# Optimization experiments

Hardware: AMD Instinct MI355X
Metric: run time of the kernel (lower is better)

The kernel has to match this reference:

```python
import jax, jax.numpy as jnp
import numpy as np

B = 262144      # points per batch
DIM = 3         # input_dim
L = 16          # levels
T = 19          # log2 hash table size
F = 2           # features per level
N_MIN, N_MAX = 16, 512

_b = np.exp((np.log(N_MAX) - np.log(N_MIN)) / (L - 1))
RES = np.floor(N_MIN * _b ** np.arange(L)).astype(np.float32).reshape(1, 1, L, 1)

# voxel corner offsets [1, DIM, 1, 2^DIM]
_border = np.empty((DIM, 2 ** DIM), dtype=np.uint32)
for i in range(DIM):
    _border[i, :] = np.array(([0] * 2 ** i + [1] * 2 ** i) * 2 ** (DIM - i - 1), dtype=np.uint32)
BORDER = _border.reshape(1, DIM, 1, 2 ** DIM)

# tiny-cuda-nn hash primes; all fit in uint32. Since the torch code takes the
# result mod 2^T (a power of two), int64 and uint32 arithmetic agree on the
# low bits, so uint32 hashing is bit-exact with the original.
PRIMES = np.array([1, 2654435761, 805459861], dtype=np.uint32)
MASK = np.uint32(2 ** T - 1)


def setup_inputs() -> dict:
    key = jax.random.key(0)
    k1, k2 = jax.random.split(key)
    x = jax.random.uniform(k1, (B, DIM), dtype=jnp.float32)  # coords in [0,1)
    tables = jax.random.uniform(k2, (L, 2 ** T, F), dtype=jnp.float32,
                                minval=-1e-4, maxval=1e-4)
    return {"x": x, "tables": tables}


def reference(x, tables):
    res = jnp.asarray(RES)                                   # [1,1,L,1]
    border = jnp.asarray(BORDER)                             # [1,DIM,1,2^DIM]
    primes = jnp.asarray(PRIMES)
    scaled = x[:, :, None, None] * res                       # [B,DIM,L,1]
    grid = jnp.floor(scaled).astype(jnp.uint32) + border     # [B,DIM,L,2^DIM]
    # spatial hash: xor of per-dim coord * prime, mod 2^T
    h = (grid[:, 0] * primes[0]) ^ (grid[:, 1] * primes[1]) ^ (grid[:, 2] * primes[2])
    idx = (h & MASK).astype(jnp.int32)                       # [B,L,2^DIM]
    gathered = tables[jnp.arange(L)[None, :, None], idx]     # [B,L,2^DIM,F]
    # multilinear interpolation weights
    w = jnp.prod(1.0 - jnp.abs(scaled - grid.astype(scaled.dtype)), axis=1)  # [B,L,2^DIM]
    out = jnp.einsum('blv,blvf->blf', w, gathered)           # [B,L,F]
    return out.reshape(x.shape[0], L * F)
```

## Files before the change

### kernel.cpp

```cpp
#include <hip/hip_runtime.h>


#define NB 262144
#define NL 16
#define TSIZE (1u << 19)
#define TMASK ((1u << 19) - 1u)
#define P1 2654435761u
#define P2 805459861u

typedef float vf2 __attribute__((ext_vector_type(2)));
typedef float vf4 __attribute__((ext_vector_type(4)));

__constant__ float RES_C[NL] = {16.f, 20.f, 25.f, 32.f, 40.f, 50.f, 64.f, 80.f,
                                101.f, 128.f, 161.f, 203.f, 256.f, 322.f, 406.f, 512.f};

__device__ __forceinline__ void ngp_point_level(
    float px, float py, float pz, int l, const float* __restrict__ tables,
    float& o0, float& o1) {
  const float res = RES_C[l];
  const float sx = px * res, sy = py * res, sz = pz * res;
  const float fx = floorf(sx), fy = floorf(sy), fz = floorf(sz);
  const unsigned ix = (unsigned)fx, iy = (unsigned)fy, iz = (unsigned)fz;

  const unsigned hy0 = iy * P1, hy1 = hy0 + P1;
  const unsigned hz0 = iz * P2, hz1 = hz0 + P2;

  const float wx0 = 1.0f - fabsf(sx - fx);
  const float wx1 = 1.0f - fabsf(sx - (fx + 1.0f));
  const float wy0 = 1.0f - fabsf(sy - fy);
  const float wy1 = 1.0f - fabsf(sy - (fy + 1.0f));
  const float wz0 = 1.0f - fabsf(sz - fz);
  const float wz1 = 1.0f - fabsf(sz - (fz + 1.0f));

  const vf2* __restrict__ tbl2 = (const vf2*)tables + (size_t)l * TSIZE;
  const vf4* __restrict__ tbl4 = (const vf4*)tables + (size_t)l * (TSIZE / 2);

  unsigned hyz[4];
  hyz[0] = hy0 ^ hz0;
  hyz[1] = hy1 ^ hz0;
  hyz[2] = hy0 ^ hz1;
  hyz[3] = hy1 ^ hz1;

  vf2 g[8];
  if ((ix & 1u) == 0u) {
#pragma unroll
    for (int p = 0; p < 4; ++p) {
      const unsigned i0 = (ix ^ hyz[p]) & TMASK;
      const vf4 q = tbl4[i0 >> 1];
      vf2 lo; lo.x = q.x; lo.y = q.y;
      vf2 hi; hi.x = q.z; hi.y = q.w;
      const bool x0_is_lo = (i0 & 1u) == 0u;
      g[2 * p + 0] = x0_is_lo ? lo : hi;
      g[2 * p + 1] = x0_is_lo ? hi : lo;
    }
  } else {
#pragma unroll
    for (int p = 0; p < 4; ++p) {
      const unsigned i0 = (ix ^ hyz[p]) & TMASK;
      const unsigned i1 = ((ix + 1u) ^ hyz[p]) & TMASK;
      g[2 * p + 0] = tbl2[i0];
      g[2 * p + 1] = tbl2[i1];
    }
  }

  o0 = 0.0f; o1 = 0.0f;
#pragma unroll
  for (int v = 0; v < 8; ++v) {
    const float w = ((v & 1) ? wx1 : wx0) * ((v & 2) ? wy1 : wy0) * ((v & 4) ? wz1 : wz0);
    o0 = fmaf(w, g[v].x, o0);
    o1 = fmaf(w, g[v].y, o1);
  }
}

__global__ __launch_bounds__(256) void ngp_gather_kernel(
    const float* __restrict__ x,
    const float* __restrict__ tables,
    vf2* __restrict__ ws) {
  const int i = blockIdx.x;
  const int lvl = (i & 7) | ((i >> 13) << 3);
  const int chunk = (i >> 3) & 1023;
  const int b = chunk * 256 + threadIdx.x;

  const float px = __builtin_nontemporal_load(x + b * 3 + 0);
  const float py = __builtin_nontemporal_load(x + b * 3 + 1);
  const float pz = __builtin_nontemporal_load(x + b * 3 + 2);

  float o0, o1;
  ngp_point_level(px, py, pz, lvl, tables, o0, o1);

  vf2 r; r.x = o0; r.y = o1;
  __builtin_nontemporal_store(r, ws + (size_t)lvl * NB + b);
}

__global__ __launch_bounds__(256) void ngp_transpose_kernel(
    const vf2* __restrict__ ws,
    vf4* __restrict__ out4) {
  __shared__ vf2 tile[NL][257];
  const int t = threadIdx.x;
  const int p0 = blockIdx.x * 256;

#pragma unroll
  for (int l = 0; l < NL; ++l) {
    tile[l][t] = __builtin_nontemporal_load(ws + (size_t)l * NB + p0 + t);
  }
  __syncthreads();

#pragma unroll
  for (int k = 0; k < 8; ++k) {
    const int q = k * 256 + t;
    const int pq = q >> 3;
    const int wq = q & 7;
    const vf2 a = tile[2 * wq + 0][pq];
    const vf2 c = tile[2 * wq + 1][pq];
    vf4 v; v.x = a.x; v.y = a.y; v.z = c.x; v.w = c.y;
    __builtin_nontemporal_store(v, out4 + (size_t)p0 * 8 + q);
  }
}

__global__ __launch_bounds__(256) void ngp_fused_kernel(
    const float* __restrict__ x, const float* __restrict__ tables,
    float* __restrict__ out) {
  const int tid = blockIdx.x * blockDim.x + threadIdx.x;
  const int l = tid & (NL - 1);
  const int b = tid >> 4;
  float o0, o1;
  ngp_point_level(x[b * 3], x[b * 3 + 1], x[b * 3 + 2], l, tables, o0, o1);
  float2 r = make_float2(o0, o1);
  ((float2*)out)[tid] = r;
}

extern "C" void kernel_launch(void* const* d_in, const int* in_sizes, int n_in,
                              void* d_out, int out_size, void* d_ws, size_t ws_size,
                              hipStream_t stream) {
  const float* x = (const float*)d_in[0];
  const float* tables = (const float*)d_in[1];
  float* out = (float*)d_out;

  const size_t ws_needed = (size_t)NL * NB * sizeof(vf2);
  if (ws_size >= ws_needed) {
    vf2* ws = (vf2*)d_ws;
    ngp_gather_kernel<<<NB * NL / 256, 256, 0, stream>>>(x, tables, ws);
    ngp_transpose_kernel<<<NB / 256, 256, 0, stream>>>(ws, (vf4*)out);
  } else {
    ngp_fused_kernel<<<NB * NL / 256, 256, 0, stream>>>(x, tables, out);
  }
}
```

Baseline: 197.7 us.

## Cache dense coarse-level grids in LDS and remap blocks per XCD

For the three coarsest levels, the block loads every grid vertex (up to 26^3) from the hash table into shared memory once, then serves 8192 points' corner lookups from LDS instead of global random gathers. The remaining levels keep the global gather path. Blocks grow to 1024 threads and are assigned so each XCD sees contiguous level/chunk work, aiming at better L2 locality per table. The cost is a large LDS footprint (~140KB) that limits occupancy, plus prefill work that is redundant across the 32 chunks of each coarse level.

```diff
diff --git a/kernel.cpp b/kernel.cpp
--- a/kernel.cpp
+++ b/kernel.cpp
@@ -7,6 +7,16 @@
 #define TMASK ((1u << 19) - 1u)
 #define P1 2654435761u
 #define P2 805459861u
+
+#define NCL 3
+#define LDS_ENT (26 * 26 * 26)
+#define CPTS 8192
+#define CBLKS (NB / CPTS)
+#define CB_PER_XCD ((NCL * CBLKS) / 8)
+#define FINE_CHUNKS 256
+#define FINE_TOTAL ((NL - NCL) * FINE_CHUNKS)
+#define FINE_PER_XCD (FINE_TOTAL / 8)
+#define GRID_BLOCKS (8 * (CB_PER_XCD + FINE_PER_XCD))
 
 typedef float vf2 __attribute__((ext_vector_type(2)));
 typedef float vf4 __attribute__((ext_vector_type(4)));
@@ -72,14 +82,101 @@
   }
 }
 
-__global__ __launch_bounds__(256) void ngp_gather_kernel(
+template <int E>
+__device__ __forceinline__ void coarse_block(
+    const int lvl, const int cchunk, const float* __restrict__ x,
+    const float* __restrict__ tables, vf2* __restrict__ ws,
+    vf2* __restrict__ cache) {
+  const int tid = threadIdx.x;
+  const vf4* __restrict__ tbl4 = (const vf4*)tables + (size_t)lvl * (TSIZE / 2);
+
+  constexpr int HE = (E + 1) / 2;
+  constexpr int U = HE * E * E;
+
+  for (int u = tid; u < U; u += 1024) {
+    const int iz = u / (HE * E);
+    const int rem = u - iz * (HE * E);
+    const int iy = rem / HE;
+    const int ixh = rem - iy * HE;
+    const unsigned ix = 2u * (unsigned)ixh;
+    const unsigned h0 = (ix ^ ((unsigned)iy * P1) ^ ((unsigned)iz * P2)) & TMASK;
+    const vf4 q = tbl4[h0 >> 1];
+    vf2 lo; lo.x = q.x; lo.y = q.y;
+    vf2 hi; hi.x = q.z; hi.y = q.w;
+    const bool x0_is_lo = (h0 & 1u) == 0u;
+    const int d0 = (int)ix + E * (iy + E * iz);
+    cache[d0] = x0_is_lo ? lo : hi;
+    if ((int)ix + 1 < E) cache[d0 + 1] = x0_is_lo ? hi : lo;
+  }
+  __syncthreads();
+
+  const float res = RES_C[lvl];
+  const int base = cchunk * CPTS;
+#pragma unroll
+  for (int k = 0; k < CPTS / 1024; ++k) {
+    const int b = base + k * 1024 + tid;
+    const float px = __builtin_nontemporal_load(x + b * 3 + 0);
+    const float py = __builtin_nontemporal_load(x + b * 3 + 1);
+    const float pz = __builtin_nontemporal_load(x + b * 3 + 2);
+
+    const float sx = px * res, sy = py * res, sz = pz * res;
+    const float fx = floorf(sx), fy = floorf(sy), fz = floorf(sz);
+    const int ix = (int)fx, iy = (int)fy, iz = (int)fz;
+
+    const float wx0 = 1.0f - fabsf(sx - fx);
+    const float wx1 = 1.0f - fabsf(sx - (fx + 1.0f));
+    const float wy0 = 1.0f - fabsf(sy - fy);
+    const float wy1 = 1.0f - fabsf(sy - (fy + 1.0f));
+    const float wz0 = 1.0f - fabsf(sz - fz);
+    const float wz1 = 1.0f - fabsf(sz - (fz + 1.0f));
+
+    const int d = ix + E * (iy + E * iz);
+    vf2 g[8];
+    g[0] = cache[d];
+    g[1] = cache[d + 1];
+    g[2] = cache[d + E];
+    g[3] = cache[d + E + 1];
+    g[4] = cache[d + E * E];
+    g[5] = cache[d + E * E + 1];
+    g[6] = cache[d + E * E + E];
+    g[7] = cache[d + E * E + E + 1];
+
+    float o0 = 0.0f, o1 = 0.0f;
+#pragma unroll
+    for (int v = 0; v < 8; ++v) {
+      const float w = ((v & 1) ? wx1 : wx0) * ((v & 2) ? wy1 : wy0) * ((v & 4) ? wz1 : wz0);
+      o0 = fmaf(w, g[v].x, o0);
+      o1 = fmaf(w, g[v].y, o1);
+    }
+    vf2 r; r.x = o0; r.y = o1;
+    __builtin_nontemporal_store(r, ws + (size_t)lvl * NB + b);
+  }
+}
+
+__global__ __launch_bounds__(1024) void ngp_gather_kernel(
     const float* __restrict__ x,
     const float* __restrict__ tables,
     vf2* __restrict__ ws) {
-  const int i = blockIdx.x;
-  const int lvl = (i & 7) | ((i >> 13) << 3);
-  const int chunk = (i >> 3) & 1023;
-  const int b = chunk * 256 + threadIdx.x;
+  __shared__ vf2 cache[LDS_ENT];
+
+  const int x8 = blockIdx.x & 7;
+  const int j = blockIdx.x >> 3;
+
+  if (j < CB_PER_XCD) {
+    const int u = x8 * CB_PER_XCD + j;
+    const int lvl = u >> 5;
+    const int cchunk = u & 31;
+    switch (lvl) {
+      case 0: coarse_block<17>(0, cchunk, x, tables, ws, cache); break;
+      case 1: coarse_block<21>(1, cchunk, x, tables, ws, cache); break;
+      default: coarse_block<26>(2, cchunk, x, tables, ws, cache); break;
+    }
+    return;
+  }
+
+  const int g = x8 * FINE_PER_XCD + (j - CB_PER_XCD);
+  const int lvl = NCL + (g >> 8);
+  const int b = (g & 255) * 1024 + threadIdx.x;
 
   const float px = __builtin_nontemporal_load(x + b * 3 + 0);
   const float py = __builtin_nontemporal_load(x + b * 3 + 1);
@@ -139,7 +236,7 @@
   const size_t ws_needed = (size_t)NL * NB * sizeof(vf2);
   if (ws_size >= ws_needed) {
     vf2* ws = (vf2*)d_ws;
-    ngp_gather_kernel<<<NB * NL / 256, 256, 0, stream>>>(x, tables, ws);
+    ngp_gather_kernel<<<GRID_BLOCKS, 1024, 0, stream>>>(x, tables, ws);
     ngp_transpose_kernel<<<NB / 256, 256, 0, stream>>>(ws, (vf4*)out);
   } else {
     ngp_fused_kernel<<<NB * NL / 256, 256, 0, stream>>>(x, tables, out);
```

Measured after the change: 190.7 us. -3.6%, faster.
